# Kernel optimization log

Measured on AMD Instinct MI355X. Metric: run time of the kernel, lower is better.

Reference implementation:

```python
import jax, jax.numpy as jnp
import numpy as np

B, S, H, N, D = 2, 2048, 1024, 16, 64  # batch, seq, hidden, heads, head_size
PAD = -30000.0


def setup_inputs() -> dict:
    key = jax.random.key(0)
    kx, kqkv, kout, krpe = jax.random.split(key, 4)
    x = jax.random.normal(kx, (B, S, H), jnp.float32)
    qkv = jax.random.normal(kqkv, (H, 3, N, D), jnp.float32) * H ** (-0.5)
    out_w = jax.random.normal(kout, (N, D, H), jnp.float32) * (N * D) ** (-0.5)
    # rpe_bias is zero-init in torch; use small randn so the bias path is exercised
    rpe_bias = jax.random.normal(krpe, (N, S), jnp.float32) * 0.02
    return {"x": x, "qkv": qkv, "out_w": out_w, "rpe_bias": rpe_bias}


def reference(x, qkv, out_w, rpe_bias):
    # q, k, v: [B, N, S, D]
    q, k, v = jnp.einsum('bsx,xMnd->Mbnsd', x, qkv)
    s = x.shape[1]
    a = jnp.einsum('bnsd,bntd->bnst', q, k) * q.shape[-1] ** (-0.5)
    # cumulative relative-position bias: bias[n, i, j] = cumsum(rpe)[n, i-j] for i>=j,
    # PAD otherwise (exactly what to_tril produces on the row-broadcast cumsum).
    cum = jnp.cumsum(rpe_bias[:, :s], axis=-1)            # [N, S]
    rel = jnp.arange(s)[:, None] - jnp.arange(s)[None, :]  # [S, S], i - j
    bias = jnp.where(rel >= 0, cum[:, jnp.clip(rel, 0)], PAD)  # [N, S, S]
    a = jax.nn.softmax(a + bias, axis=-1)
    mix = jnp.einsum('bnst,bntd->bnsd', a, v)
    return jnp.einsum('bnsd,ndx->bsx', mix, out_w)
```

## Files before the change

kernel.cpp:

```cpp
#include <hip/hip_runtime.h>
#include <hip/hip_bf16.h>
#include <cstdint>
#include <cstddef>

#define B_   2
#define S_   2048
#define H_   1024
#define NH   16
#define DH   64
#define SCALE 0.125f

typedef __hip_bfloat16 bf16;
typedef short bf16x8 __attribute__((ext_vector_type(8)));
typedef float f32x4 __attribute__((ext_vector_type(4)));

#define MFMA16(a, b, c) __builtin_amdgcn_mfma_f32_16x16x32_bf16((a), (b), (c), 0, 0, 0)

__device__ __forceinline__ void async16(const void* g, void* l) {
  __builtin_amdgcn_global_load_lds(
      (const __attribute__((address_space(1))) void*)g,
      (__attribute__((address_space(3))) void*)l,
      16, 0, 0);
}

__global__ void convert_f32_bf16(const float* __restrict__ src, bf16* __restrict__ dst,
                                 int n) {
  int i = (blockIdx.x * 256 + threadIdx.x) * 4;
  if (i + 3 < n) {
    float4 v = *(const float4*)(src + i);
    dst[i + 0] = __float2bfloat16(v.x);
    dst[i + 1] = __float2bfloat16(v.y);
    dst[i + 2] = __float2bfloat16(v.z);
    dst[i + 3] = __float2bfloat16(v.w);
  }
}

__global__ void transpose_f32_bf16(const float* __restrict__ src, bf16* __restrict__ dst,
                                   int R, int C) {
  __shared__ bf16 tile[32][33];
  int c0 = blockIdx.x * 32, r0 = blockIdx.y * 32;
  int tx = threadIdx.x & 31, ty = threadIdx.x >> 5;
  for (int i = 0; i < 32; i += 8)
    tile[ty + i][tx] = __float2bfloat16(src[(size_t)(r0 + ty + i) * C + c0 + tx]);
  __syncthreads();
  for (int i = 0; i < 32; i += 8)
    dst[(size_t)(c0 + ty + i) * R + r0 + tx] = tile[tx][ty + i];
}

__global__ void rpe_scan(const float* __restrict__ rpe, float* __restrict__ cum) {
  __shared__ float ssum[256];
  int n = blockIdx.x, t = threadIdx.x;
  float loc[8];
  float s = 0.f;
  int base = t * 8;
  for (int u = 0; u < 8; ++u) {
    loc[u] = rpe[n * S_ + base + u];
    s += loc[u];
  }
  ssum[t] = s;
  __syncthreads();
  float own = s;
  for (int off = 1; off < 256; off <<= 1) {
    float v = (t >= off) ? ssum[t - off] : 0.f;
    __syncthreads();
    ssum[t] += v;
    __syncthreads();
  }
  float run = ssum[t] - own;
  for (int u = 0; u < 8; ++u) {
    run += loc[u];
    cum[n * S_ + base + u] = run;
  }
}

template <int MODE>
__global__ __launch_bounds__(256, 2)
void gemm_bt(const bf16* __restrict__ A, const bf16* __restrict__ Bt,
             bf16* __restrict__ C0, bf16* __restrict__ C1, bf16* __restrict__ C2,
             float* __restrict__ F0) {
  __shared__ bf16 As[128 * 32] __attribute__((aligned(16)));
  __shared__ bf16 Bs[128 * 32] __attribute__((aligned(16)));
  const int tid = threadIdx.x, lane = tid & 63, w = tid >> 6;
  const int lr = lane & 15, lq = lane >> 4;
  const int m0 = blockIdx.y * 128, n0 = blockIdx.x * 128;
  const int wm = (w & 1) * 64, wn = (w >> 1) * 64;

  f32x4 acc[4][4] = {};

  for (int k0 = 0; k0 < 1024; k0 += 32) {
    __syncthreads();
    for (int t = 0; t < 2; ++t) {
      int c = (t * 4 + w) * 64 + lane;
      int row = c >> 2, ch = c & 3;
      int k8 = (ch ^ ((row >> 1) & 3)) * 8;
      async16(A + (size_t)(m0 + row) * 1024 + k0 + k8,
              (char*)As + (size_t)(t * 4 + w) * 1024 + lane * 16);
      async16(Bt + (size_t)(n0 + row) * 1024 + k0 + k8,
              (char*)Bs + (size_t)(t * 4 + w) * 1024 + lane * 16);
    }
    __syncthreads();
    bf16x8 af[4], bfr[4];
#pragma unroll
    for (int mt = 0; mt < 4; ++mt) {
      int row = wm + mt * 16 + lr;
      af[mt] = *(const bf16x8*)(As + row * 32 + ((lq ^ ((row >> 1) & 3)) << 3));
    }
#pragma unroll
    for (int nt = 0; nt < 4; ++nt) {
      int row = wn + nt * 16 + lr;
      bfr[nt] = *(const bf16x8*)(Bs + row * 32 + ((lq ^ ((row >> 1) & 3)) << 3));
    }
#pragma unroll
    for (int mt = 0; mt < 4; ++mt)
#pragma unroll
      for (int nt = 0; nt < 4; ++nt)
        acc[mt][nt] = MFMA16(af[mt], bfr[nt], acc[mt][nt]);
  }

  if (MODE == 0) {
#pragma unroll
    for (int nt = 0; nt < 4; ++nt) {
      int cN = n0 + wn + nt * 16 + lr;
      int mm = cN >> 10, nn = (cN >> 6) & 15, dd = cN & 63;
      if (mm < 2) {
        bf16* dst = mm == 0 ? C0 : C1;
#pragma unroll
        for (int mt = 0; mt < 4; ++mt)
#pragma unroll
          for (int r = 0; r < 4; ++r) {
            int rM = m0 + wm + mt * 16 + lq * 4 + r;
            int bb = rM >> 11, ss = rM & 2047;
            dst[((size_t)(bb * NH + nn) * S_ + ss) * DH + dd] =
                __float2bfloat16(acc[mt][nt][r]);
          }
      } else {
#pragma unroll
        for (int mt = 0; mt < 4; ++mt)
#pragma unroll
          for (int r = 0; r < 4; ++r) {
            int rM = m0 + wm + mt * 16 + lq * 4 + r;
            int bb = rM >> 11, ss = rM & 2047;
            C2[((size_t)(bb * NH + nn) * DH + dd) * S_ + ss] =
                __float2bfloat16(acc[mt][nt][r]);
          }
      }
    }
  } else {
#pragma unroll
    for (int mt = 0; mt < 4; ++mt)
#pragma unroll
      for (int nt = 0; nt < 4; ++nt)
#pragma unroll
        for (int r = 0; r < 4; ++r) {
          int rM = m0 + wm + mt * 16 + lq * 4 + r;
          int cN = n0 + wn + nt * 16 + lr;
          F0[(size_t)rM * 1024 + cN] = acc[mt][nt][r];
        }
  }
}

__global__ __launch_bounds__(256, 4)
void fa_kernel(const bf16* __restrict__ q, const bf16* __restrict__ k,
               const bf16* __restrict__ vt, const float* __restrict__ cum,
               bf16* __restrict__ mix) {
  __shared__ char smem[34816] __attribute__((aligned(16)));
  bf16* Ps = (bf16*)smem;
  float* cumbuf = (float*)(smem + 33792);

  const int tid = threadIdx.x, lane = tid & 63, w = tid >> 6;
  const int lr = lane & 15, lq = lane >> 4;

  const int L = blockIdx.x;
  const int xcd = L & 7, slot = L >> 3;
  const int bn = xcd + 8 * (slot >> 5);
  const int ti = 31 - (slot & 31);
  const int n = bn & (NH - 1);
  const int b = bn >> 4;
  const float* cumn = cum + n * S_;

  const int i0 = ti * 64;
  const int nj = (ti >> 1) + 1;

  const bf16* qbase = q + ((size_t)bn * S_ + i0 + w * 16) * DH;
  bf16x8 qf[2];
#pragma unroll
  for (int kt = 0; kt < 2; ++kt)
    qf[kt] = *(const bf16x8*)(qbase + lr * DH + kt * 32 + lq * 8);

  f32x4 oacc[4] = {};
  float m_i = -1e30f, l_i = 0.f;
  const int iloc = w * 16 + lr;

  for (int jt = 0; jt < nj; ++jt) {
    const int j0 = jt * 128;
    const bool diag = (jt == nj - 1);
    __syncthreads();

    const char* ksrc = (const char*)(k + ((size_t)bn * S_ + j0) * DH);
#pragma unroll
    for (int t = 0; t < 4; ++t) {
      int cb = t * 4 + w;
      int row = cb * 8 + (lane >> 3);
      int cs = (lane & 7) ^ (row & 7);
      async16(ksrc + row * 128 + cs * 16, smem + cb * 1024 + lane * 16);
    }
    const char* vsrc = (const char*)(vt + (size_t)bn * DH * S_);
#pragma unroll
    for (int t = 0; t < 4; ++t) {
      int cb = t * 4 + w;
      int row = cb * 4 + (lane >> 4);
      int cs = (lane & 15) ^ (row & 15);
      async16(vsrc + (size_t)row * (S_ * 2) + j0 * 2 + cs * 16,
              smem + 17408 + cb * 1024 + lane * 16);
    }
    {
      int src = i0 - j0 - 127 + tid;
      src = src < 0 ? 0 : (src > S_ - 1 ? S_ - 1 : src);
      cumbuf[tid] = cumn[src];
    }
    __syncthreads();

    f32x4 sa[8] = {};
#pragma unroll
    for (int kt = 0; kt < 2; ++kt)
#pragma unroll
      for (int nt = 0; nt < 8; ++nt) {
        int krow = nt * 16 + lr;
        bf16x8 kf = *(const bf16x8*)(smem + krow * 128 +
                        (((kt * 4 + lq) ^ (krow & 7)) << 4));
        sa[nt] = MFMA16(kf, qf[kt], sa[nt]);
      }
    __syncthreads();

    const int doff = i0 - j0;
    float rmax = -1e30f;
    if (!diag) {
#pragma unroll
      for (int nt = 0; nt < 8; ++nt)
#pragma unroll
        for (int r = 0; r < 4; ++r) {
          int rel = iloc - nt * 16 - lq * 4 - r;
          float val = sa[nt][r] * SCALE + cumbuf[127 + rel];
          sa[nt][r] = val;
          rmax = fmaxf(rmax, val);
        }
    } else {
#pragma unroll
      for (int nt = 0; nt < 8; ++nt)
#pragma unroll
        for (int r = 0; r < 4; ++r) {
          int rel = iloc - nt * 16 - lq * 4 - r;
          float val = (doff + rel >= 0) ? sa[nt][r] * SCALE + cumbuf[127 + rel]
                                        : -1e30f;
          sa[nt][r] = val;
          rmax = fmaxf(rmax, val);
        }
    }
    float mx = fmaxf(rmax, __shfl_xor(rmax, 16));
    mx = fmaxf(mx, __shfl_xor(mx, 32));
    float newm = fmaxf(m_i, mx);
    float al = __expf(m_i - newm);
    m_i = newm;
    float rs = 0.f;
#pragma unroll
    for (int nt = 0; nt < 8; ++nt)
#pragma unroll
      for (int r = 0; r < 4; ++r) {
        float p = __expf(sa[nt][r] - newm);
        sa[nt][r] = p;
        rs += p;
      }
    rs += __shfl_xor(rs, 16);
    rs += __shfl_xor(rs, 32);
    l_i = l_i * al + rs;
    float alr[4];
#pragma unroll
    for (int r = 0; r < 4; ++r) alr[r] = __shfl(al, lq * 4 + r);
#pragma unroll
    for (int dt = 0; dt < 4; ++dt)
#pragma unroll
      for (int r = 0; r < 4; ++r) oacc[dt][r] *= alr[r];

#pragma unroll
    for (int nt = 0; nt < 8; ++nt) {
      bf16 pk[4];
#pragma unroll
      for (int r = 0; r < 4; ++r) pk[r] = __float2bfloat16(sa[nt][r]);
      *(uint64_t*)(Ps + iloc * 136 + nt * 16 + lq * 4) = *(const uint64_t*)pk;
    }

#pragma unroll
    for (int kt2 = 0; kt2 < 4; ++kt2) {
      bf16x8 pf = *(const bf16x8*)(Ps + (w * 16 + lr) * 136 + kt2 * 32 + lq * 8);
#pragma unroll
      for (int dt = 0; dt < 4; ++dt) {
        int vrow = dt * 16 + lr;
        bf16x8 vf = *(const bf16x8*)(smem + 17408 + vrow * 256 +
                        (((kt2 * 4 + lq) ^ (vrow & 15)) << 4));
        oacc[dt] = MFMA16(pf, vf, oacc[dt]);
      }
    }
  }

  float lr4[4];
#pragma unroll
  for (int r = 0; r < 4; ++r) lr4[r] = __shfl(l_i, lq * 4 + r);
#pragma unroll
  for (int dt = 0; dt < 4; ++dt)
#pragma unroll
    for (int r = 0; r < 4; ++r) {
      int i = i0 + w * 16 + lq * 4 + r;
      int d = dt * 16 + lr;
      mix[((size_t)(b * S_ + i) * NH + n) * DH + d] =
          __float2bfloat16(oacc[dt][r] / lr4[r]);
    }
}

extern "C" void kernel_launch(void* const* d_in, const int* in_sizes, int n_in,
                              void* d_out, int out_size, void* d_ws, size_t ws_size,
                              hipStream_t stream) {
  const float* x     = (const float*)d_in[0];
  const float* qkv   = (const float*)d_in[1];
  const float* out_w = (const float*)d_in[2];
  const float* rpe   = (const float*)d_in[3];
  float* out = (float*)d_out;

  char* ws = (char*)d_ws;
  bf16* qkvT  = (bf16*)(ws + 0);
  bf16* outwT = (bf16*)(ws + 6291456);
  bf16* xb    = (bf16*)(ws + 8388608);
  bf16* qb    = (bf16*)(ws + 16777216);
  bf16* kb    = (bf16*)(ws + 25165824);
  bf16* vtb   = (bf16*)(ws + 33554432);
  bf16* mixb  = (bf16*)(ws + 41943040);
  float* cum  = (float*)(ws + 50331648);

  convert_f32_bf16<<<4096, 256, 0, stream>>>(x, xb, 4096 * 1024);
  transpose_f32_bf16<<<dim3(3072 / 32, 1024 / 32), 256, 0, stream>>>(qkv, qkvT, 1024, 3072);
  transpose_f32_bf16<<<dim3(1024 / 32, 1024 / 32), 256, 0, stream>>>(out_w, outwT, 1024, 1024);
  rpe_scan<<<NH, 256, 0, stream>>>(rpe, cum);
  gemm_bt<0><<<dim3(3072 / 128, 4096 / 128), 256, 0, stream>>>(xb, qkvT, qb, kb, vtb, nullptr);
  fa_kernel<<<1024, 256, 0, stream>>>(qb, kb, vtb, cum, mixb);
  gemm_bt<1><<<dim3(1024 / 128, 4096 / 128), 256, 0, stream>>>(mixb, outwT, nullptr, nullptr, nullptr, out);
}
```

Baseline: 214.6 us.

## Stage QKV GEMM epilogue through LDS for coalesced stores; separate P buffer in attention

The QKV projection epilogue now writes each wave's 64x64 tile into padded LDS (transposed for the V^T output) and then issues coalesced 16-byte global stores, replacing scattered 2-byte writes. The flash-attention kernel gives P its own LDS region instead of aliasing the K tile. That lets it drop the barrier between the QK^T MFMAs and the softmax. In exchange the attention kernel's LDS grows to about 50KB and its launch bound falls from 4 to 3 blocks per CU, which may reduce occupancy.

```diff
diff --git a/kernel.cpp b/kernel.cpp
--- a/kernel.cpp
+++ b/kernel.cpp
@@ -78,8 +78,9 @@
 void gemm_bt(const bf16* __restrict__ A, const bf16* __restrict__ Bt,
              bf16* __restrict__ C0, bf16* __restrict__ C1, bf16* __restrict__ C2,
              float* __restrict__ F0) {
-  __shared__ bf16 As[128 * 32] __attribute__((aligned(16)));
-  __shared__ bf16 Bs[128 * 32] __attribute__((aligned(16)));
+  __shared__ char smem[MODE == 0 ? 36864 : 16384] __attribute__((aligned(16)));
+  bf16* As = (bf16*)smem;
+  bf16* Bs = (bf16*)(smem + 8192);
   const int tid = threadIdx.x, lane = tid & 63, w = tid >> 6;
   const int lr = lane & 15, lq = lane >> 4;
   const int m0 = blockIdx.y * 128, n0 = blockIdx.x * 128;
@@ -118,31 +119,46 @@
   }
 
   if (MODE == 0) {
-#pragma unroll
-    for (int nt = 0; nt < 4; ++nt) {
-      int cN = n0 + wn + nt * 16 + lr;
-      int mm = cN >> 10, nn = (cN >> 6) & 15, dd = cN & 63;
-      if (mm < 2) {
-        bf16* dst = mm == 0 ? C0 : C1;
-#pragma unroll
-        for (int mt = 0; mt < 4; ++mt)
-#pragma unroll
-          for (int r = 0; r < 4; ++r) {
-            int rM = m0 + wm + mt * 16 + lq * 4 + r;
-            int bb = rM >> 11, ss = rM & 2047;
-            dst[((size_t)(bb * NH + nn) * S_ + ss) * DH + dd] =
+    __syncthreads();
+    bf16* E = (bf16*)smem + w * (64 * 72);
+    const int cbase = n0 + wn;
+    const int mm = cbase >> 10, nn = (cbase >> 6) & 15;
+    const int bb = (m0 + wm) >> 11;
+    const int sbase = (m0 + wm) & 2047;
+    if (mm < 2) {
+#pragma unroll
+      for (int mt = 0; mt < 4; ++mt)
+#pragma unroll
+        for (int nt = 0; nt < 4; ++nt)
+#pragma unroll
+          for (int r = 0; r < 4; ++r)
+            E[(mt * 16 + lq * 4 + r) * 72 + nt * 16 + lr] =
                 __float2bfloat16(acc[mt][nt][r]);
-          }
-      } else {
-#pragma unroll
-        for (int mt = 0; mt < 4; ++mt)
-#pragma unroll
-          for (int r = 0; r < 4; ++r) {
-            int rM = m0 + wm + mt * 16 + lq * 4 + r;
-            int bb = rM >> 11, ss = rM & 2047;
-            C2[((size_t)(bb * NH + nn) * DH + dd) * S_ + ss] =
+      bf16* dst = (mm == 0 ? C0 : C1) +
+                  ((size_t)(bb * NH + nn) * S_ + sbase) * DH;
+#pragma unroll
+      for (int it = 0; it < 8; ++it) {
+        int c = it * 64 + lane;
+        int rw = c >> 3, c8 = c & 7;
+        *(uint4*)(dst + (size_t)rw * DH + c8 * 8) =
+            *(const uint4*)(E + rw * 72 + c8 * 8);
+      }
+    } else {
+#pragma unroll
+      for (int mt = 0; mt < 4; ++mt)
+#pragma unroll
+        for (int nt = 0; nt < 4; ++nt)
+#pragma unroll
+          for (int r = 0; r < 4; ++r)
+            E[(nt * 16 + lr) * 72 + mt * 16 + lq * 4 + r] =
                 __float2bfloat16(acc[mt][nt][r]);
-          }
+      bf16* dst = C2 + (size_t)(bb * NH + nn) * DH * S_;
+#pragma unroll
+      for (int it = 0; it < 8; ++it) {
+        int c = it * 64 + lane;
+        int dr = c >> 3, c8 = c & 7;
+        *(uint4*)(dst + (size_t)dr * S_ + sbase + c8 * 8) =
+            *(const uint4*)(E + dr * 72 + c8 * 8);
       }
     }
   } else {
@@ -159,13 +175,13 @@
   }
 }
 
-__global__ __launch_bounds__(256, 4)
+__global__ __launch_bounds__(256, 3)
 void fa_kernel(const bf16* __restrict__ q, const bf16* __restrict__ k,
                const bf16* __restrict__ vt, const float* __restrict__ cum,
                bf16* __restrict__ mix) {
-  __shared__ char smem[34816] __attribute__((aligned(16)));
-  bf16* Ps = (bf16*)smem;
-  float* cumbuf = (float*)(smem + 33792);
+  __shared__ char smem[51200] __attribute__((aligned(16)));
+  bf16* Ps = (bf16*)(smem + 32768);
+  float* cumbuf = (float*)(smem + 50176);
 
   const int tid = threadIdx.x, lane = tid & 63, w = tid >> 6;
   const int lr = lane & 15, lq = lane >> 4;
@@ -211,7 +227,7 @@
       int row = cb * 4 + (lane >> 4);
       int cs = (lane & 15) ^ (row & 15);
       async16(vsrc + (size_t)row * (S_ * 2) + j0 * 2 + cs * 16,
-              smem + 17408 + cb * 1024 + lane * 16);
+              smem + 16384 + cb * 1024 + lane * 16);
     }
     {
       int src = i0 - j0 - 127 + tid;
@@ -230,7 +246,6 @@
                         (((kt * 4 + lq) ^ (krow & 7)) << 4));
         sa[nt] = MFMA16(kf, qf[kt], sa[nt]);
       }
-    __syncthreads();
 
     const int doff = i0 - j0;
     float rmax = -1e30f;
@@ -295,7 +310,7 @@
 #pragma unroll
       for (int dt = 0; dt < 4; ++dt) {
         int vrow = dt * 16 + lr;
-        bf16x8 vf = *(const bf16x8*)(smem + 17408 + vrow * 256 +
+        bf16x8 vf = *(const bf16x8*)(smem + 16384 + vrow * 256 +
                         (((kt2 * 4 + lq) ^ (vrow & 15)) << 4));
         oacc[dt] = MFMA16(pf, vf, oacc[dt]);
       }
```

After: 200.2 us. 1.07x faster.
